# Optimization experiments

Hardware: AMD Instinct MI355X
Metric: run time of the kernel (lower is better)

## Reference

```python
import jax, jax.numpy as jnp
import numpy as np
import math

N_CELLS = 16384
INPUT_DIM = 512
HIDDEN = 512


def build_neighbors(n):
    n_bits = max(1, int(math.ceil(math.log2(n))))
    idx = np.arange(n)
    flips = [idx ^ (1 << b) for b in range(n_bits)]
    ring = [(idx + 1) % n, (idx - 1) % n]
    allnb = np.stack(flips + ring, axis=1)
    # dedupe per row; for power-of-2 n every row has exactly n_bits+1 uniques
    rows = [sorted(set(r.tolist())) for r in allnb]
    return np.asarray(rows, dtype=np.int32)


def setup_inputs() -> dict:
    key = jax.random.key(0)
    ks = jax.random.split(key, 12)
    n, d, h = N_CELLS, INPUT_DIM, HIDDEN
    amp = jax.random.uniform(ks[0], (n, h)) * 0.5 + 0.5
    phase = jax.random.normal(ks[1], (n, h)) * 0.3 + (2 * math.pi * jnp.arange(n) / n)[:, None]
    return {
        "x": jax.random.normal(ks[2], (1, d), dtype=jnp.float32),
        "pump_W": jax.random.normal(ks[3], (n, d), dtype=jnp.float32) / np.sqrt(d),
        "pump_b": jax.random.normal(ks[4], (n,), dtype=jnp.float32) * 0.01,
        "dec_W": jax.random.normal(ks[5], (d, 2 * h), dtype=jnp.float32) / np.sqrt(2 * h),
        "dec_b": jax.random.normal(ks[6], (d,), dtype=jnp.float32) * 0.01,
        "cs_re": (amp * jnp.cos(phase)).astype(jnp.float32),
        "cs_im": (amp * jnp.sin(phase)).astype(jnp.float32),
        "excited": jax.random.uniform(ks[7], (n,)) * 0.6,  # some cells above 0.5 threshold
        "phase_vel": jax.random.normal(ks[8], (n, h), dtype=jnp.float32) * 0.05,
        "cav_re": jax.random.normal(ks[9], (h,), dtype=jnp.float32) * 0.01,
        "cav_im": jax.random.normal(ks[10], (h,), dtype=jnp.float32) * 0.01,
        "neighbors": jnp.asarray(build_neighbors(n)),
    }


def reference(x, pump_W, pump_b, dec_W, dec_b, cs_re, cs_im, excited, phase_vel, cav_re, cav_im, neighbors):
    states = (cs_re + 1j * cs_im).astype(jnp.complex64)          # [n,h]
    cavity = (cav_re + 1j * cav_im).astype(jnp.complex64)        # [h]

    # pump + excited fraction update
    pump = jax.nn.sigmoid(x @ pump_W.T + pump_b)[0]              # [n]
    excited = jnp.clip(excited * 0.95 + pump * 0.05, 0.0, 1.0)

    # free phase rotation: polar(1, 0.1*phase_vel)
    states = states * jnp.exp(1j * (phase_vel * 0.1)).astype(jnp.complex64)

    # neighbor phase coupling (hypercube + ring, k=15 neighbors each)
    ang = jnp.angle(states)                                      # [n,h]
    nb_states = states[neighbors]                                # [n,k,h]
    coupling = jnp.cos(ang[:, None, :] - ang[neighbors])         # [n,k,h]
    interference = 0.1 * jnp.sum(coupling * nb_states, axis=1)   # [n,h]
    k = neighbors.shape[1]
    new_states = 0.7 * states + 0.3 * interference / k

    # lasing: population inversion threshold
    lasing = excited > 0.5                                       # [n]
    n_lasing = jnp.sum(lasing)
    maskf = lasing.astype(jnp.float32)[:, None]
    # emission uses pre-phase-lock states (torch copies lasing_cells first)
    emission = jnp.sum(new_states * maskf, axis=0) / jnp.maximum(n_lasing, 1).astype(jnp.float32)
    cavity_new = jnp.where(n_lasing > 0, 0.8 * cavity + 0.2 * emission, cavity)

    # phase-lock lasing cells to (old) cavity phase
    cavity_phase = jnp.angle(cavity)                             # old cavity
    new_ang = jnp.angle(new_states)
    locked = 0.3 * cavity_phase[None, :] + 0.7 * new_ang
    locked_states = jnp.abs(new_states) * jnp.exp(1j * locked)
    new_states = jnp.where(lasing[:, None], locked_states.astype(jnp.complex64), new_states)
    excited = jnp.where(lasing, excited * 0.9, excited * 0.98)

    # cavity feedback (updated cavity) + amplitude renorm
    new_states = new_states + 0.05 * cavity_new[None, :]
    amp = jnp.abs(new_states)
    amp = amp / (jnp.max(amp, axis=-1, keepdims=True) + 1e-8)
    final_states = (amp * jnp.exp(1j * jnp.angle(new_states))).astype(jnp.complex64)

    # decode cavity mode
    out_real = jnp.concatenate([cavity_new.real, cavity_new.imag])[None, :].astype(jnp.float32)  # [1,2h]
    pred = out_real @ dec_W.T + dec_b                            # [1, input_dim]
    tension = jnp.var(jnp.abs(final_states))
    return pred, tension
```

## Files before the change

### kernel.cpp

```cpp
#include <hip/hip_runtime.h>
#include <hip/hip_fp16.h>
#include <math.h>

#define N_CELLS 16384
#define HID 512
#define IND 512

#define ROT_BLOCKS  2048
#define PUMP_BLOCKS 4096

#define CPB 16
#define CELL_BLOCKS (N_CELLS / CPB)
#define PRED_BLOCKS 128

#define CNT_OFF   0
#define EMIS_OFF  128
#define LAS_OFF   8192
#define VPART_OFF (LAS_OFF + N_CELLS*4)
#define ROT_OFF   (1<<20)
#define NST_OFF   (ROT_OFF + (size_t)N_CELLS*HID*4)

typedef unsigned int u32;

__device__ inline __half2 u2h(u32 u) { union { u32 u; __half2 h; } x; x.u = u; return x.h; }
__device__ inline u32 h2u(__half2 h) { union { u32 u; __half2 h; } x; x.h = h; return x.u; }
__device__ inline u32 packh2(float re, float im) { return h2u(__floats2half2_rn(re, im)); }
__device__ inline float2 unph2(u32 u) { __half2 h = u2h(u); return make_float2(__low2float(h), __high2float(h)); }

#if __has_builtin(__builtin_amdgcn_fdot2)
typedef _Float16 hv2 __attribute__((ext_vector_type(2)));
__device__ inline float dot2u(u32 a, u32 b) {
    union { u32 u; hv2 h; } x, y; x.u = a; y.u = b;
    return __builtin_amdgcn_fdot2(x.h, y.h, 0.f, false);
}
#else
__device__ inline float dot2u(u32 a, u32 b) {
    float2 af = unph2(a), bf = unph2(b);
    return fmaf(af.x, bf.x, af.y * bf.y);
}
#endif

__device__ inline void accnb(__half2& acc, u32 y, u32 q) {
    float d = dot2u(y, q);
    acc = __hfma2(__float2half2_rn(d), u2h(q), acc);
}

__device__ inline u32 fincell(u32 y, __half2 acc, int las, float& emR, float& emI) {
    float2 yf = unph2(y);
    float a  = fmaf(yf.x, yf.x, yf.y * yf.y);
    float rs = rsqrtf(a);
    float sq = a * rs;
    float2 af = make_float2(__low2float(acc), __high2float(acc));
    float nr = 0.7f * sq * yf.x + 0.002f * rs * af.x;
    float ni = 0.7f * sq * yf.y + 0.002f * rs * af.y;
    if (las) { emR += nr; emI += ni; }
    return packh2(nr, ni);
}

__device__ inline u32 rot1(float re, float im, float w) {
    float sc = rsqrtf(sqrtf(fmaf(re, re, im * im)));
    float s, c;
    __sincosf(0.1f * w, &s, &c);
    return packh2((re * c - im * s) * sc, (re * s + im * c) * sc);
}

__global__ __launch_bounds__(256) void k_front(const float* __restrict__ cr,
        const float* __restrict__ ci, const float* __restrict__ pv,
        u32* __restrict__ yt,
        const float* __restrict__ x, const float* __restrict__ pW,
        const float* __restrict__ pb, const float* __restrict__ excited,
        int* __restrict__ lasing, int* __restrict__ cnt) {
    int b = blockIdx.x, tid = threadIdx.x;
    if (b < ROT_BLOCKS) {
        __shared__ u32 tile[64 * 65];
        int cb = b >> 3, hb = b & 7;
        const float4* cr4 = (const float4*)cr;
        const float4* ci4 = (const float4*)ci;
        const float4* pv4 = (const float4*)pv;
#pragma unroll
        for (int j = 0; j < 4; ++j) {
            int idx = tid + 256 * j;
            int row = idx >> 4, c4 = idx & 15;
            size_t g = (size_t)(cb * 64 + row) * 128 + hb * 16 + c4;
            float4 a = cr4[g], bi = ci4[g], w = pv4[g];
            u32* dst = &tile[row * 65 + (c4 << 2)];
            dst[0] = rot1(a.x, bi.x, w.x);
            dst[1] = rot1(a.y, bi.y, w.y);
            dst[2] = rot1(a.z, bi.z, w.z);
            dst[3] = rot1(a.w, bi.w, w.w);
        }
        if (b == 0 && tid == 0) *cnt = 0;
        __syncthreads();
#pragma unroll
        for (int j = 0; j < 4; ++j) {
            int idx = tid + 256 * j;
            int chr = idx >> 4, c4 = idx & 15;
            uint4 v;
            v.x = tile[(c4 * 4 + 0) * 65 + chr];
            v.y = tile[(c4 * 4 + 1) * 65 + chr];
            v.z = tile[(c4 * 4 + 2) * 65 + chr];
            v.w = tile[(c4 * 4 + 3) * 65 + chr];
            ((uint4*)(yt + (size_t)(hb * 64 + chr) * N_CELLS + cb * 64))[c4] = v;
        }
    } else {
        int gtid = (b - ROT_BLOCKS) * 256 + tid;
        int cell = gtid >> 6, lane = gtid & 63;
        const float4* w4 = (const float4*)(pW + (size_t)cell * IND);
        const float4* x4 = (const float4*)x;
        float acc = 0.f;
#pragma unroll
        for (int q = 0; q < 2; ++q) {
            float4 a = w4[lane + 64 * q];
            float4 bx = x4[lane + 64 * q];
            acc += a.x * bx.x + a.y * bx.y + a.z * bx.z + a.w * bx.w;
        }
#pragma unroll
        for (int o = 32; o; o >>= 1) acc += __shfl_xor(acc, o, 64);
        if (lane == 0) {
            float p = 1.f / (1.f + expf(-(acc + pb[cell])));
            float e = excited[cell] * 0.95f + p * 0.05f;
            e = fminf(fmaxf(e, 0.f), 1.f);
            lasing[cell] = (e > 0.5f) ? 1 : 0;
        }
    }
}

__global__ __launch_bounds__(256) void k_coup(const u32* __restrict__ yt,
                                              const int* __restrict__ lasv,
                                              u32* __restrict__ nstT,
                                              float2* __restrict__ emisT) {
    __shared__ __align__(16) u32 col[N_CELLS];
    int ch = blockIdx.x, tid = threadIdx.x;
    const uint4* src = (const uint4*)(yt + (size_t)ch * N_CELLS);
    uint4* cdst = (uint4*)col;
#pragma unroll
    for (int k = 0; k < 16; ++k) cdst[tid + 256 * k] = src[tid + 256 * k];
    __syncthreads();

    float emR = 0.f, emI = 0.f;
    uint4* outp = (uint4*)(nstT + (size_t)ch * N_CELLS);
    const int4* l4 = (const int4*)lasv;
#pragma unroll 2
    for (int j = 0; j < 16; ++j) {
        int s = tid + 256 * j;
        int c = s << 2;
        uint4 sq = *(const uint4*)&col[c];
        __half2 z = __floats2half2_rn(0.f, 0.f);
        __half2 a0 = z, a1 = z, a2 = z, a3 = z;
#pragma unroll
        for (int bb = 2; bb < 14; ++bb) {
            uint4 q = *(const uint4*)&col[c ^ (1 << bb)];
            accnb(a0, sq.x, q.x);
            accnb(a1, sq.y, q.y);
            accnb(a2, sq.z, q.z);
            accnb(a3, sq.w, q.w);
        }
        u32 qm = col[(c - 1) & (N_CELLS - 1)];
        u32 qp = col[(c + 4) & (N_CELLS - 1)];
        accnb(a0, sq.x, sq.y); accnb(a0, sq.x, sq.z); accnb(a0, sq.x, qm);
        accnb(a1, sq.y, sq.x); accnb(a1, sq.y, sq.w); accnb(a1, sq.y, sq.z);
        accnb(a2, sq.z, sq.w); accnb(a2, sq.z, sq.x); accnb(a2, sq.z, sq.y);
        accnb(a3, sq.w, sq.z); accnb(a3, sq.w, sq.y); accnb(a3, sq.w, qp);
        int4 lv = l4[s];
        uint4 ov;
        ov.x = fincell(sq.x, a0, lv.x, emR, emI);
        ov.y = fincell(sq.y, a1, lv.y, emR, emI);
        ov.z = fincell(sq.z, a2, lv.z, emR, emI);
        ov.w = fincell(sq.w, a3, lv.w, emR, emI);
        outp[s] = ov;
    }
    __syncthreads();
#pragma unroll
    for (int o = 32; o; o >>= 1) { emR += __shfl_xor(emR, o, 64); emI += __shfl_xor(emI, o, 64); }
    float* scr = (float*)col;
    int wid = tid >> 6, lane = tid & 63;
    if (lane == 0) { scr[wid] = emR; scr[4 + wid] = emI; }
    __syncthreads();
    if (tid == 0)
        emisT[ch] = make_float2(scr[0] + scr[1] + scr[2] + scr[3],
                                scr[4] + scr[5] + scr[6] + scr[7]);
}

__global__ __launch_bounds__(256) void k_finall(const u32* __restrict__ nstT,
        const int* __restrict__ lasv, const float2* __restrict__ emisT,
        const float* __restrict__ cavr, const float* __restrict__ cavi,
        const float* __restrict__ dW, const float* __restrict__ db,
        float2* __restrict__ vpart, int* __restrict__ cnt,
        float* __restrict__ out) {
    __shared__ __align__(16) float sout[1024];
    __shared__ float sphase[512];
    __shared__ int ic[4];
    __shared__ int snl;
    __shared__ float wmax[4][16];
    __shared__ float w1[4], w2[4];
    __shared__ int slast;
    __shared__ double l1s[4], l2s[4];

    int t = threadIdx.x, wid = t >> 6, lane = t & 63;

    const int4* l4 = (const int4*)lasv;
    int n = 0;
#pragma unroll
    for (int k = 0; k < 16; ++k) {
        int4 v = l4[t + 256 * k];
        n += v.x + v.y + v.z + v.w;
    }
#pragma unroll
    for (int o = 32; o; o >>= 1) n += __shfl_xor(n, o, 64);
    if (lane == 0) ic[wid] = n;
    __syncthreads();
    if (t == 0) snl = ic[0] + ic[1] + ic[2] + ic[3];
    __syncthreads();
    int nl = snl;
    float inv = (nl > 0) ? 0.2f / (float)nl : 0.f;
#pragma unroll
    for (int k = 0; k < 2; ++k) {
        int i = t + 256 * k;
        float crv = cavr[i], civ = cavi[i];
        float2 e = emisT[i];
        sout[i]       = (nl > 0) ? 0.8f * crv + e.x * inv : crv;
        sout[512 + i] = (nl > 0) ? 0.8f * civ + e.y * inv : civ;
        sphase[i] = atan2f(civ, crv);
    }
    __syncthreads();

    int b = blockIdx.x;
    if (b < CELL_BLOCKS) {
        int cell = b * CPB + (t & 15);
        int chs = t >> 4;
        int lasc = lasv[cell];
        float amps[32];
        float mx = 0.f;
#pragma unroll
        for (int k = 0; k < 32; ++k) {
            int ch = chs + 16 * k;
            float2 vf = unph2(nstT[(size_t)ch * N_CELLS + cell]);
            float vx = vf.x, vy = vf.y;
            if (lasc) {
                float r = sqrtf(fmaf(vx, vx, vy * vy));
                float lk = 0.3f * sphase[ch] + 0.7f * atan2f(vy, vx);
                float sn, cs;
                __sincosf(lk, &sn, &cs);
                vx = r * cs; vy = r * sn;
            }
            vx += 0.05f * sout[ch];
            vy += 0.05f * sout[512 + ch];
            float a = sqrtf(fmaf(vx, vx, vy * vy));
            amps[k] = a;
            mx = fmaxf(mx, a);
        }
        mx = fmaxf(mx, __shfl_xor(mx, 16, 64));
        mx = fmaxf(mx, __shfl_xor(mx, 32, 64));
        if (lane < 16) wmax[wid][lane] = mx;
        __syncthreads();
        mx = fmaxf(fmaxf(wmax[0][t & 15], wmax[1][t & 15]),
                   fmaxf(wmax[2][t & 15], wmax[3][t & 15]));
        float invm = 1.f / (mx + 1e-8f);
        float s1 = 0.f, s2 = 0.f;
#pragma unroll
        for (int k = 0; k < 32; ++k) {
            float a = amps[k] * invm;
            s1 += a;
            s2 += a * a;
        }
#pragma unroll
        for (int o = 32; o; o >>= 1) { s1 += __shfl_xor(s1, o, 64); s2 += __shfl_xor(s2, o, 64); }
        if (lane == 0) { w1[wid] = s1; w2[wid] = s2; }
        __syncthreads();
        if (t == 0) {
            vpart[b] = make_float2(w1[0] + w1[1] + w1[2] + w1[3],
                                   w2[0] + w2[1] + w2[2] + w2[3]);
            __threadfence();
            int old = atomicAdd(cnt, 1);
            slast = (old == CELL_BLOCKS - 1) ? 1 : 0;
        }
        __syncthreads();
        if (slast) {
            __threadfence();
            double d1 = (double)vpart[t].x + (double)vpart[t + 256].x
                      + (double)vpart[t + 512].x + (double)vpart[t + 768].x;
            double d2 = (double)vpart[t].y + (double)vpart[t + 256].y
                      + (double)vpart[t + 512].y + (double)vpart[t + 768].y;
#pragma unroll
            for (int o = 32; o; o >>= 1) { d1 += __shfl_xor(d1, o, 64); d2 += __shfl_xor(d2, o, 64); }
            if (lane == 0) { l1s[wid] = d1; l2s[wid] = d2; }
            __syncthreads();
            if (t == 0) {
                double t1 = l1s[0] + l1s[1] + l1s[2] + l1s[3];
                double t2 = l2s[0] + l2s[1] + l2s[2] + l2s[3];
                double nn = (double)N_CELLS * (double)HID;
                double mean = t1 / nn;
                out[IND] = (float)(t2 / nn - mean * mean);
            }
        }
    } else {
        int j = (b - CELL_BLOCKS) * 4 + wid;
        const float4* w4 = (const float4*)(dW + (size_t)j * (2 * HID));
        const float4* o4 = (const float4*)sout;
        float a2 = 0.f;
#pragma unroll
        for (int tt = 0; tt < 4; ++tt) {
            float4 a = w4[lane + 64 * tt];
            float4 bx = o4[lane + 64 * tt];
            a2 += a.x * bx.x + a.y * bx.y + a.z * bx.z + a.w * bx.w;
        }
#pragma unroll
        for (int o = 32; o; o >>= 1) a2 += __shfl_xor(a2, o, 64);
        if (lane == 0) out[j] = a2 + db[j];
    }
}

extern "C" void kernel_launch(void* const* d_in, const int* in_sizes, int n_in,
                              void* d_out, int out_size, void* d_ws, size_t ws_size,
                              hipStream_t stream) {
    const float* x       = (const float*)d_in[0];
    const float* pump_W  = (const float*)d_in[1];
    const float* pump_b  = (const float*)d_in[2];
    const float* dec_W   = (const float*)d_in[3];
    const float* dec_b   = (const float*)d_in[4];
    const float* cs_re   = (const float*)d_in[5];
    const float* cs_im   = (const float*)d_in[6];
    const float* excited = (const float*)d_in[7];
    const float* pvel    = (const float*)d_in[8];
    const float* cav_re  = (const float*)d_in[9];
    const float* cav_im  = (const float*)d_in[10];

    float* out = (float*)d_out;
    char* ws = (char*)d_ws;
    int*    cnt   = (int*)(ws + CNT_OFF);
    float2* emisT = (float2*)(ws + EMIS_OFF);
    int*    lasv  = (int*)(ws + LAS_OFF);
    float2* vpart = (float2*)(ws + VPART_OFF);
    u32*    yt    = (u32*)(ws + ROT_OFF);
    u32*    nstT  = (u32*)(ws + NST_OFF);

    k_front<<<ROT_BLOCKS + PUMP_BLOCKS, 256, 0, stream>>>(
        cs_re, cs_im, pvel, yt, x, pump_W, pump_b, excited, lasv, cnt);
    k_coup<<<HID, 256, 0, stream>>>(yt, lasv, nstT, emisT);
    k_finall<<<CELL_BLOCKS + PRED_BLOCKS, 256, 0, stream>>>(
        nstT, lasv, emisT, cav_re, cav_im, dec_W, dec_b, vpart, cnt, out);
}
```

Baseline: 271.6 us.

## Compute cavity update once in coupling kernel and tile final pass through LDS

The last coupling block, found with an atomic counter, now computes the lasing count, the updated cavity and the cavity phase once and writes them to workspace. Previously every final-pass block re-read the 16K-entry lasing vector and recomputed these values. The final kernel now stages a 16-cell by 512-channel tile into swizzled shared memory with vectorized loads, replacing strided scalar gathers. It also computes sum, sum of squares and max in one pass without a 32-entry register array. This adds a second counter and a last-block tail in the coupling kernel, and relies on the algebraic rescaling of the sums by the inverse max.

After: 265.2 us. 1.02x faster.

```diff
diff --git a/kernel.cpp b/kernel.cpp
--- a/kernel.cpp
+++ b/kernel.cpp
@@ -15,7 +15,8 @@
 
 #define CNT_OFF   0
 #define EMIS_OFF  128
-#define LAS_OFF   8192
+#define CAV_OFF   4352
+#define LAS_OFF   16384
 #define VPART_OFF (LAS_OFF + N_CELLS*4)
 #define ROT_OFF   (1<<20)
 #define NST_OFF   (ROT_OFF + (size_t)N_CELLS*HID*4)
@@ -89,7 +90,7 @@
             dst[2] = rot1(a.z, bi.z, w.z);
             dst[3] = rot1(a.w, bi.w, w.w);
         }
-        if (b == 0 && tid == 0) *cnt = 0;
+        if (b == 0 && tid == 0) { cnt[0] = 0; cnt[1] = 0; }
         __syncthreads();
 #pragma unroll
         for (int j = 0; j < 4; ++j) {
@@ -128,7 +129,11 @@
 __global__ __launch_bounds__(256) void k_coup(const u32* __restrict__ yt,
                                               const int* __restrict__ lasv,
                                               u32* __restrict__ nstT,
-                                              float2* __restrict__ emisT) {
+                                              float2* __restrict__ emisT,
+                                              const float* __restrict__ cavr,
+                                              const float* __restrict__ cavi,
+                                              float* __restrict__ cavws,
+                                              int* __restrict__ cnt) {
     __shared__ __align__(16) u32 col[N_CELLS];
     int ch = blockIdx.x, tid = threadIdx.x;
     const uint4* src = (const uint4*)(yt + (size_t)ch * N_CELLS);
@@ -138,6 +143,7 @@
     __syncthreads();
 
     float emR = 0.f, emI = 0.f;
+    int nlo = 0;
     uint4* outp = (uint4*)(nstT + (size_t)ch * N_CELLS);
     const int4* l4 = (const int4*)lasv;
 #pragma unroll 2
@@ -162,6 +168,7 @@
         accnb(a2, sq.z, sq.w); accnb(a2, sq.z, sq.x); accnb(a2, sq.z, sq.y);
         accnb(a3, sq.w, sq.z); accnb(a3, sq.w, sq.y); accnb(a3, sq.w, qp);
         int4 lv = l4[s];
+        nlo += lv.x + lv.y + lv.z + lv.w;
         uint4 ov;
         ov.x = fincell(sq.x, a0, lv.x, emR, emI);
         ov.y = fincell(sq.y, a1, lv.y, emR, emI);
@@ -171,107 +178,115 @@
     }
     __syncthreads();
 #pragma unroll
-    for (int o = 32; o; o >>= 1) { emR += __shfl_xor(emR, o, 64); emI += __shfl_xor(emI, o, 64); }
+    for (int o = 32; o; o >>= 1) {
+        emR += __shfl_xor(emR, o, 64);
+        emI += __shfl_xor(emI, o, 64);
+        nlo += __shfl_xor(nlo, o, 64);
+    }
     float* scr = (float*)col;
+    int* iscr = (int*)col;
     int wid = tid >> 6, lane = tid & 63;
-    if (lane == 0) { scr[wid] = emR; scr[4 + wid] = emI; }
+    if (lane == 0) { scr[wid] = emR; scr[4 + wid] = emI; iscr[8 + wid] = nlo; }
     __syncthreads();
-    if (tid == 0)
+    if (tid == 0) {
         emisT[ch] = make_float2(scr[0] + scr[1] + scr[2] + scr[3],
                                 scr[4] + scr[5] + scr[6] + scr[7]);
+        __threadfence();
+        int old = atomicAdd(cnt, 1);
+        iscr[12] = (old == HID - 1) ? 1 : 0;
+    }
+    __syncthreads();
+    if (iscr[12]) {
+        __threadfence();
+        int nl = iscr[8] + iscr[9] + iscr[10] + iscr[11];
+        float inv = (nl > 0) ? 0.2f / (float)nl : 0.f;
+#pragma unroll
+        for (int k2 = 0; k2 < 2; ++k2) {
+            int i = tid + 256 * k2;
+            float crv = cavr[i], civ = cavi[i];
+            float2 e = emisT[i];
+            cavws[i]        = (nl > 0) ? 0.8f * crv + e.x * inv : crv;
+            cavws[512 + i]  = (nl > 0) ? 0.8f * civ + e.y * inv : civ;
+            cavws[1024 + i] = atan2f(civ, crv);
+        }
+    }
 }
 
 __global__ __launch_bounds__(256) void k_finall(const u32* __restrict__ nstT,
-        const int* __restrict__ lasv, const float2* __restrict__ emisT,
-        const float* __restrict__ cavr, const float* __restrict__ cavi,
+        const int* __restrict__ lasv, const float* __restrict__ cavws,
         const float* __restrict__ dW, const float* __restrict__ db,
-        float2* __restrict__ vpart, int* __restrict__ cnt,
+        float2* __restrict__ vpart, int* __restrict__ cnt2,
         float* __restrict__ out) {
-    __shared__ __align__(16) float sout[1024];
-    __shared__ float sphase[512];
-    __shared__ int ic[4];
-    __shared__ int snl;
-    __shared__ float wmax[4][16];
-    __shared__ float w1[4], w2[4];
-    __shared__ int slast;
-    __shared__ double l1s[4], l2s[4];
-
-    int t = threadIdx.x, wid = t >> 6, lane = t & 63;
-
-    const int4* l4 = (const int4*)lasv;
-    int n = 0;
-#pragma unroll
-    for (int k = 0; k < 16; ++k) {
-        int4 v = l4[t + 256 * k];
-        n += v.x + v.y + v.z + v.w;
-    }
-#pragma unroll
-    for (int o = 32; o; o >>= 1) n += __shfl_xor(n, o, 64);
-    if (lane == 0) ic[wid] = n;
-    __syncthreads();
-    if (t == 0) snl = ic[0] + ic[1] + ic[2] + ic[3];
-    __syncthreads();
-    int nl = snl;
-    float inv = (nl > 0) ? 0.2f / (float)nl : 0.f;
-#pragma unroll
-    for (int k = 0; k < 2; ++k) {
-        int i = t + 256 * k;
-        float crv = cavr[i], civ = cavi[i];
-        float2 e = emisT[i];
-        sout[i]       = (nl > 0) ? 0.8f * crv + e.x * inv : crv;
-        sout[512 + i] = (nl > 0) ? 0.8f * civ + e.y * inv : civ;
-        sphase[i] = atan2f(civ, crv);
-    }
-    __syncthreads();
-
-    int b = blockIdx.x;
+    int b = blockIdx.x, t = threadIdx.x;
+    int wid = t >> 6, lane = t & 63;
     if (b < CELL_BLOCKS) {
-        int cell = b * CPB + (t & 15);
-        int chs = t >> 4;
-        int lasc = lasv[cell];
-        float amps[32];
-        float mx = 0.f;
-#pragma unroll
-        for (int k = 0; k < 32; ++k) {
-            int ch = chs + 16 * k;
-            float2 vf = unph2(nstT[(size_t)ch * N_CELLS + cell]);
+        __shared__ __align__(16) u32 tile[CPB * HID];
+        __shared__ __align__(16) float scav[1536];
+        __shared__ float w1[4], w2[4];
+        __shared__ int slast;
+        __shared__ double l1s[4], l2s[4];
+
+        const float4* c4p = (const float4*)cavws;
+#pragma unroll
+        for (int k2 = 0; k2 < 2; ++k2) {
+            int i = t + 256 * k2;
+            if (i < 384) ((float4*)scav)[i] = c4p[i];
+        }
+        int c0 = b * CPB;
+#pragma unroll
+        for (int j = 0; j < 8; ++j) {
+            int idx = t + 256 * j;
+            int ch = idx >> 2, q = idx & 3;
+            uint4 v = ((const uint4*)(nstT + (size_t)ch * N_CELLS + c0))[q];
+#pragma unroll
+            for (int e = 0; e < 4; ++e) {
+                int cell = q * 4 + e;
+                int sw = ch ^ (((e ^ q) & 1) << 4);
+                tile[cell * HID + sw] = ((const u32*)&v)[e];
+            }
+        }
+        __syncthreads();
+
+        int cell = t >> 4, kk = t & 15;
+        int lasc = lasv[c0 + cell];
+        int swb = ((cell ^ (cell >> 2)) & 1) << 4;
+        const u32* trow = &tile[cell * HID];
+        float sa = 0.f, sa2 = 0.f, mx = 0.f;
+#pragma unroll 8
+        for (int i = 0; i < 32; ++i) {
+            int ch = kk + 16 * i;
+            float2 vf = unph2(trow[ch ^ swb]);
             float vx = vf.x, vy = vf.y;
             if (lasc) {
                 float r = sqrtf(fmaf(vx, vx, vy * vy));
-                float lk = 0.3f * sphase[ch] + 0.7f * atan2f(vy, vx);
+                float lk = 0.3f * scav[1024 + ch] + 0.7f * atan2f(vy, vx);
                 float sn, cs;
                 __sincosf(lk, &sn, &cs);
                 vx = r * cs; vy = r * sn;
             }
-            vx += 0.05f * sout[ch];
-            vy += 0.05f * sout[512 + ch];
-            float a = sqrtf(fmaf(vx, vx, vy * vy));
-            amps[k] = a;
-            mx = fmaxf(mx, a);
-        }
-        mx = fmaxf(mx, __shfl_xor(mx, 16, 64));
-        mx = fmaxf(mx, __shfl_xor(mx, 32, 64));
-        if (lane < 16) wmax[wid][lane] = mx;
-        __syncthreads();
-        mx = fmaxf(fmaxf(wmax[0][t & 15], wmax[1][t & 15]),
-                   fmaxf(wmax[2][t & 15], wmax[3][t & 15]));
+            vx += 0.05f * scav[ch];
+            vy += 0.05f * scav[512 + ch];
+            float a2v = fmaf(vx, vx, vy * vy);
+            float a = sqrtf(a2v);
+            sa += a; sa2 += a2v; mx = fmaxf(mx, a);
+        }
+#pragma unroll
+        for (int o = 1; o < 16; o <<= 1) {
+            sa += __shfl_xor(sa, o, 64);
+            sa2 += __shfl_xor(sa2, o, 64);
+            mx = fmaxf(mx, __shfl_xor(mx, o, 64));
+        }
         float invm = 1.f / (mx + 1e-8f);
-        float s1 = 0.f, s2 = 0.f;
-#pragma unroll
-        for (int k = 0; k < 32; ++k) {
-            float a = amps[k] * invm;
-            s1 += a;
-            s2 += a * a;
-        }
-#pragma unroll
-        for (int o = 32; o; o >>= 1) { s1 += __shfl_xor(s1, o, 64); s2 += __shfl_xor(s2, o, 64); }
+        float s1 = sa * invm, s2 = sa2 * invm * invm;
+        s1 += __shfl_xor(s1, 16, 64); s2 += __shfl_xor(s2, 16, 64);
+        s1 += __shfl_xor(s1, 32, 64); s2 += __shfl_xor(s2, 32, 64);
         if (lane == 0) { w1[wid] = s1; w2[wid] = s2; }
         __syncthreads();
         if (t == 0) {
             vpart[b] = make_float2(w1[0] + w1[1] + w1[2] + w1[3],
                                    w2[0] + w2[1] + w2[2] + w2[3]);
             __threadfence();
-            int old = atomicAdd(cnt, 1);
+            int old = atomicAdd(cnt2, 1);
             slast = (old == CELL_BLOCKS - 1) ? 1 : 0;
         }
         __syncthreads();
@@ -296,7 +311,7 @@
     } else {
         int j = (b - CELL_BLOCKS) * 4 + wid;
         const float4* w4 = (const float4*)(dW + (size_t)j * (2 * HID));
-        const float4* o4 = (const float4*)sout;
+        const float4* o4 = (const float4*)cavws;
         float a2 = 0.f;
 #pragma unroll
         for (int tt = 0; tt < 4; ++tt) {
@@ -329,6 +344,7 @@
     char* ws = (char*)d_ws;
     int*    cnt   = (int*)(ws + CNT_OFF);
     float2* emisT = (float2*)(ws + EMIS_OFF);
+    float*  cavws = (float*)(ws + CAV_OFF);
     int*    lasv  = (int*)(ws + LAS_OFF);
     float2* vpart = (float2*)(ws + VPART_OFF);
     u32*    yt    = (u32*)(ws + ROT_OFF);
@@ -336,7 +352,7 @@
 
     k_front<<<ROT_BLOCKS + PUMP_BLOCKS, 256, 0, stream>>>(
         cs_re, cs_im, pvel, yt, x, pump_W, pump_b, excited, lasv, cnt);
-    k_coup<<<HID, 256, 0, stream>>>(yt, lasv, nstT, emisT);
+    k_coup<<<HID, 256, 0, stream>>>(yt, lasv, nstT, emisT, cav_re, cav_im, cavws, cnt);
     k_finall<<<CELL_BLOCKS + PRED_BLOCKS, 256, 0, stream>>>(
-        nstT, lasv, emisT, cav_re, cav_im, dec_W, dec_b, vpart, cnt, out);
-}
+        nstT, lasv, cavws, dec_W, dec_b, vpart, cnt + 1, out);
+}
```
